# Kernel tuning notes

Hardware: AMD Instinct MI355X
Metric: run time of the kernel (lower is better)

Reference implementation:

```python
import jax, jax.numpy as jnp
import numpy as np
import math

N_HEAD = 12
BLOCK = 256  # local attention block size (ls)
EPS = 1e-6


def _rotate(x):
    # pairs (a, b) -> (-b, a) over last dim (matches rotate_embeddings)
    a = x[..., 0::2]
    b = x[..., 1::2]
    return jnp.stack([-b, a], axis=-1).reshape(x.shape)


def setup_inputs() -> dict:
    key = jax.random.key(0)
    k1, k2, k3 = jax.random.split(key, 3)
    B, T, C = 4, 8192, 768
    s = 0.02
    return {
        "x": jax.random.normal(k1, (B, T, C), jnp.float32),
        "w_qkv": jax.random.normal(k2, (C, 3 * C), jnp.float32) * s,
        "w_ln": jnp.ones((C,), jnp.float32),
        "w_proj": jax.random.normal(k3, (C, C), jnp.float32) * s,
    }


def reference(x, w_qkv, w_ln, w_proj):
    B, T, C = x.shape
    nh, ls = N_HEAD, BLOCK
    hd = C // nh
    ng = T // ls

    xb = x.reshape(B, ng, ls, C)
    qkv = xb @ w_qkv                                   # (B,ng,ls,3C)
    q, k, v = jnp.split(qkv, 3, axis=-1)

    # QK RMSNorm over full embedding dim (before head split)
    def rms(t):
        return t * jax.lax.rsqrt(jnp.mean(t * t, axis=-1, keepdims=True) + EPS) * w_ln
    q, k = rms(q), rms(k)

    # split heads: (B,ng,nh,ls,hd)
    def heads(t):
        return jnp.swapaxes(t.reshape(B, ng, ls, nh, hd), 2, 3)
    q, k, v = heads(q), heads(k), heads(v)

    # RoPE (repo layout: freqs tiled via cat((ts,ts)), interleaved pair rotation)
    pos = 10000.0 ** ((-2.0 * jnp.arange(0, hd, 2, dtype=jnp.float32) - 1.0) / hd)
    ts = jnp.arange(ls, dtype=jnp.float32)[:, None] * pos[None, :]   # (ls, hd/2)
    rot = jnp.concatenate([ts, ts], axis=-1)                          # (ls, hd)
    cos, sin = jnp.cos(rot), jnp.sin(rot)
    q = q * cos + _rotate(q) * sin
    k = k * cos + _rotate(k) * sin

    # block-causal scores: causal only within each local block
    scale = 1.0 / math.sqrt(hd)
    att = jnp.einsum('bgnqd,bgnkd->bgnqk', q, k) * scale              # (B,ng,nh,ls,ls)
    mask = jnp.tril(jnp.ones((ls, ls), dtype=bool))
    att = jnp.where(mask, att, -jnp.finfo(att.dtype).max)
    att = jax.nn.softmax(att, axis=-1)
    y = jnp.einsum('bgnqk,bgnkd->bgnqd', att, v)                      # (B,ng,nh,ls,hd)

    y = jnp.swapaxes(y, 2, 3).reshape(B, ng, ls, C)
    y = y @ w_proj
    return y.reshape(B, T, C)
```

## Files before the change

kernel.cpp:

```cpp
#include <hip/hip_runtime.h>
#include <math.h>

typedef __attribute__((ext_vector_type(8))) short bf16x8;
typedef __attribute__((ext_vector_type(4))) short bf16x4;
typedef __attribute__((ext_vector_type(2))) short bf16x2;
typedef __attribute__((ext_vector_type(4))) float f32x4;
typedef __attribute__((ext_vector_type(16))) float f32x16;

#define NH 12
#define HD 64
#define C0 768
#define C3 2304
#define LS 256
#define KT12 12

static __device__ __forceinline__ float bf2f(short u) {
  union { unsigned int i; float f; } c;
  c.i = ((unsigned int)(unsigned short)u) << 16;
  return c.f;
}
static __device__ __forceinline__ short f2bf(float f) {
  union { float f; unsigned int i; } c; c.f = f;
  unsigned int x = c.i;
  x += 0x7fffu + ((x >> 16) & 1u);
  return (short)(x >> 16);
}
static __device__ __forceinline__ unsigned pk2(float a, float b) {
  return (unsigned)(unsigned short)f2bf(a) | ((unsigned)(unsigned short)f2bf(b) << 16);
}

static __device__ __forceinline__ void gload_lds16(const short* g, const short* l) {
  unsigned long long ga = (unsigned long long)g;
  unsigned int la = (unsigned int)(unsigned long long)l;
  __builtin_amdgcn_global_load_lds(
      (const __attribute__((address_space(1))) void*)ga,
      (__attribute__((address_space(3))) void*)la, 16, 0, 0);
}

__global__ __launch_bounds__(256) void cast_kernel(const float* __restrict__ in,
                                                   short* __restrict__ out, int nquads) {
  int i = blockIdx.x * blockDim.x + threadIdx.x;
  int stride = gridDim.x * blockDim.x;
  for (; i < nquads; i += stride) {
    float4 v = ((const float4*)in)[i];
    bf16x4 o = { f2bf(v.x), f2bf(v.y), f2bf(v.z), f2bf(v.w) };
    ((bf16x4*)out)[i] = o;
  }
}

__global__ __launch_bounds__(256) void cast_transpose_kernel(const float* __restrict__ in,
                                                             short* __restrict__ out,
                                                             int K, int N) {
  __shared__ float tile[32][33];
  int n0 = blockIdx.x * 32, k0 = blockIdx.y * 32;
  int tx = threadIdx.x & 31, ty = threadIdx.x >> 5;
#pragma unroll
  for (int i = 0; i < 32; i += 8)
    tile[ty + i][tx] = in[(long)(k0 + ty + i) * N + n0 + tx];
  __syncthreads();
#pragma unroll
  for (int i = 0; i < 32; i += 8)
    out[(long)(n0 + ty + i) * K + k0 + tx] = f2bf(tile[tx][ty + i]);
}

template <int WNG>
__global__ __launch_bounds__(256) void cast_pack_B_kernel(const float* __restrict__ w,
                                                          short* __restrict__ Bpk, int N) {
  __shared__ short sb[WNG * 64 * 64];
  int bn = blockIdx.x, kt = blockIdx.y, t = threadIdx.x;
#pragma unroll
  for (int i = 0; i < WNG * 2; ++i) {
    int seg = i * 256 + t;
    int k = seg / (WNG * 8);
    int nc = (seg % (WNG * 8)) * 8;
    const float* src = w + ((long)(kt * 64 + k)) * N + bn * (WNG * 64) + nc;
    float4 v0 = *(const float4*)src;
    float4 v1 = *(const float4*)(src + 4);
    sb[(nc + 0) * 64 + k] = f2bf(v0.x); sb[(nc + 1) * 64 + k] = f2bf(v0.y);
    sb[(nc + 2) * 64 + k] = f2bf(v0.z); sb[(nc + 3) * 64 + k] = f2bf(v0.w);
    sb[(nc + 4) * 64 + k] = f2bf(v1.x); sb[(nc + 5) * 64 + k] = f2bf(v1.y);
    sb[(nc + 6) * 64 + k] = f2bf(v1.z); sb[(nc + 7) * 64 + k] = f2bf(v1.w);
  }
  __syncthreads();
#pragma unroll
  for (int i = 0; i < WNG * 2; ++i) {
    int c = i * 256 + t;
    int l = c & 63, f = c >> 6;
    int ks = f & 3, nt = (f >> 2) & 1, wng = f >> 3;
    int col = wng * 64 + nt * 32 + (l & 31);
    int kk = ks * 16 + (l >> 5) * 8;
    bf16x8 v = *(bf16x8*)&sb[col * 64 + kk];
    *(bf16x8*)&Bpk[(((long)bn * KT12 + kt) * (WNG * 512) + c) * 8] = v;
  }
}

__global__ void rope_tab_kernel(float* __restrict__ cost, float* __restrict__ sint) {
  int t = blockIdx.x, d = threadIdx.x;
  int i = d & 31;
  float freq = powf(10000.0f, -(float)(4 * i + 1) / 64.0f);
  float th = (float)t * freq;
  cost[t * 64 + d] = cosf(th);
  sint[t * 64 + d] = sinf(th);
}

#define PH_PRE                                         \
  __builtin_amdgcn_s_barrier();                        \
  __builtin_amdgcn_s_setprio(1);
#define PH_POST                                        \
  __builtin_amdgcn_s_setprio(0);                       \
  asm volatile("s_waitcnt lgkmcnt(0)" ::: "memory");   \
  __builtin_amdgcn_s_barrier();
#define PH_POSTV                                       \
  __builtin_amdgcn_s_setprio(0);                       \
  asm volatile("s_waitcnt lgkmcnt(0)" ::: "memory");   \
  asm volatile("s_waitcnt vmcnt(4)" ::: "memory");     \
  __builtin_amdgcn_s_barrier();
#define MMQ(MH, NP)                                                                \
  { _Pragma("unroll") for (int f_ = 0; f_ < 4; ++f_)                               \
      _Pragma("unroll") for (int n_ = 0; n_ < 2; ++n_)                             \
        _Pragma("unroll") for (int k_ = 0; k_ < 2; ++k_)                           \
          acc[(MH)*4 + f_][(NP)*2 + n_] = __builtin_amdgcn_mfma_f32_16x16x32_bf16( \
              af[f_*2 + k_], bfv[((NP)*2 + n_)*2 + k_],                            \
              acc[(MH)*4 + f_][(NP)*2 + n_], 0, 0, 0); }

template <int OUT_F32>
__global__ __launch_bounds__(512, 2) void gemm8p_kernel(const short* __restrict__ A,
                                                        const short* __restrict__ Bt,
                                                        void* __restrict__ Cout,
                                                        int N, int K, int nbn) {
  __shared__ short lds[65536];
  int t = threadIdx.x, lane = t & 63, wave = t >> 6;
  int lr = lane & 15, lg = lane >> 4;
  int wm = (wave >> 2) * 128, wn = (wave & 3) * 64;
  int id = blockIdx.x;
  int cpx = gridDim.x >> 3;
  int sw = (id & 7) * cpx + (id >> 3);
  int bm = sw / nbn, bn = sw % nbn;
  const short* Abase = A + (long)bm * 256 * K;
  const short* Bbase = Bt + (long)bn * 256 * K;
  int srow = t >> 3;
  int scol = ((t & 7) ^ (srow & 7)) * 8;
  int smax = K >> 4;

  f32x4 acc[8][4];
#pragma unroll
  for (int m = 0; m < 8; ++m)
#pragma unroll
    for (int n = 0; n < 4; ++n) acc[m][n] = (f32x4){0.f, 0.f, 0.f, 0.f};

  bf16x8 af[8], bfv[8];

  auto STAGE = [&](int s) {
    int slot = s & 3;
    int Tg = (s < smax) ? (s >> 2) : 0;
    const short* base = (slot & 2) ? Abase : Bbase;
    const short* g = base + (long)((slot & 1) * 128 + srow) * K + Tg * 64 + scol;
    int lb = ((s >> 2) & 1) * 32768 + ((slot >> 1) ^ 1) * 16384 + (slot & 1) * 8192 + t * 8;
    gload_lds16(g, &lds[lb]);
    gload_lds16(g + (long)64 * K, &lds[lb + 4096]);
  };
  auto LDA = [&](int b, int mh) {
#pragma unroll
    for (int f = 0; f < 4; ++f) {
      int R = wm + mh * 64 + f * 16 + lr;
      int rb = b * 32768 + R * 64;
      int s8 = R & 7;
      af[f * 2 + 0] = *(bf16x8*)&lds[rb + ((lg ^ s8) << 3)];
      af[f * 2 + 1] = *(bf16x8*)&lds[rb + (((4 + lg) ^ s8) << 3)];
    }
  };
  auto LDB = [&](int b, int nh) {
#pragma unroll
    for (int j = 0; j < 2; ++j) {
      int R = wn + (nh * 2 + j) * 16 + lr;
      int rb = b * 32768 + 16384 + R * 64;
      int s8 = R & 7;
      bfv[(nh * 2 + j) * 2 + 0] = *(bf16x8*)&lds[rb + ((lg ^ s8) << 3)];
      bfv[(nh * 2 + j) * 2 + 1] = *(bf16x8*)&lds[rb + (((4 + lg) ^ s8) << 3)];
    }
  };

  STAGE(0); STAGE(1); STAGE(2); STAGE(3); STAGE(4); STAGE(5);
  asm volatile("s_waitcnt vmcnt(4)" ::: "memory");
  __builtin_amdgcn_s_barrier();

  int iters = K >> 7;
  for (int i = 0; i < iters; ++i) {
    int si = 8 * i + 6;
    LDA(0, 0); LDB(0, 0);
    STAGE(si + 0);
    PH_PRE; MMQ(0, 0); PH_POST;
    LDB(0, 1);
    STAGE(si + 1);
    PH_PRE; MMQ(0, 1); PH_POST;
    LDA(0, 1);
    STAGE(si + 2);
    PH_PRE; MMQ(1, 0); PH_POST;
    STAGE(si + 3);
    PH_PRE; MMQ(1, 1); PH_POSTV;
    LDA(1, 0); LDB(1, 0);
    STAGE(si + 4);
    PH_PRE; MMQ(0, 0); PH_POST;
    LDB(1, 1);
    STAGE(si + 5);
    PH_PRE; MMQ(0, 1); PH_POST;
    LDA(1, 1);
    STAGE(si + 6);
    PH_PRE; MMQ(1, 0); PH_POST;
    STAGE(si + 7);
    PH_PRE; MMQ(1, 1); PH_POSTV;
  }

  long crow0 = (long)bm * 256 + wm;
  long ccol0 = (long)bn * 256 + wn;
#pragma unroll
  for (int f = 0; f < 8; ++f)
#pragma unroll
    for (int n = 0; n < 4; ++n)
#pragma unroll
      for (int r = 0; r < 4; ++r) {
        long row = crow0 + (f >> 2) * 64 + (f & 3) * 16 + lg * 4 + r;
        long col = ccol0 + n * 16 + lr;
        float v = acc[f][n][r];
        if (OUT_F32) ((float*)Cout)[row * N + col] = v;
        else ((short*)Cout)[row * N + col] = f2bf(v);
      }
}

template <int OUT_F32>
__global__ __launch_bounds__(256, 2) void gemm128_kernel(const short* __restrict__ Arm,
                                                         const short* __restrict__ Bpk,
                                                         void* __restrict__ Cout,
                                                         int N, int K, int nbn) {
  __shared__ short lds[32768];
  int t = threadIdx.x, lane = t & 63, wave = t >> 6;
  int wm = (wave >> 1) * 64, wng = wave & 1;
  int id = blockIdx.x;
  int cpx = gridDim.x >> 3;
  int sw = (id & 7) * cpx + (id >> 3);
  int bm = sw / nbn, bn = sw % nbn;
  int l31 = lane & 31, lh = lane >> 5;

  f32x16 acc[2][2];
#pragma unroll
  for (int m = 0; m < 2; ++m)
#pragma unroll
    for (int n = 0; n < 2; ++n)
#pragma unroll
      for (int r = 0; r < 16; ++r) acc[m][n][r] = 0.f;

  auto STAGE = [&](int T) {
    int bb = (T & 1) * 16384;
#pragma unroll
    for (int i = 0; i < 4; ++i) {
      int q = i * 256 + t;
      int row = q >> 3, cp = q & 7;
      const short* ga = Arm + ((long)(bm * 128 + row)) * K + T * 64 + ((cp ^ (row & 7)) * 8);
      gload_lds16(ga, &lds[bb + q * 8]);
      const short* gb = Bpk + ((long)bn * KT12 + T) * 8192 + (long)q * 8;
      gload_lds16(gb, &lds[bb + 8192 + q * 8]);
    }
  };

  STAGE(0);
  asm volatile("s_waitcnt vmcnt(0)" ::: "memory");
  __builtin_amdgcn_s_barrier();

  for (int T = 0; T < KT12; ++T) {
    int bb = (T & 1) * 16384;
    if (T + 1 < KT12) STAGE(T + 1);
    bf16x8 a[2][4], b[2][4];
#pragma unroll
    for (int mt = 0; mt < 2; ++mt) {
      int row = wm + mt * 32 + l31;
      int s8 = row & 7;
#pragma unroll
      for (int ks = 0; ks < 4; ++ks) {
        int g = (ks * 2 + lh) ^ s8;
        a[mt][ks] = *(bf16x8*)&lds[bb + row * 64 + g * 8];
      }
    }
#pragma unroll
    for (int nt = 0; nt < 2; ++nt)
#pragma unroll
      for (int ks = 0; ks < 4; ++ks)
        b[nt][ks] = *(bf16x8*)&lds[bb + 8192 + (((wng * 2 + nt) * 4 + ks) * 64 + lane) * 8];
    __builtin_amdgcn_s_setprio(1);
#pragma unroll
    for (int mt = 0; mt < 2; ++mt)
#pragma unroll
      for (int nt = 0; nt < 2; ++nt)
#pragma unroll
        for (int ks = 0; ks < 4; ++ks)
          acc[mt][nt] = __builtin_amdgcn_mfma_f32_32x32x16_bf16(a[mt][ks], b[nt][ks],
                                                                acc[mt][nt], 0, 0, 0);
    __builtin_amdgcn_s_setprio(0);
    asm volatile("s_waitcnt lgkmcnt(0)" ::: "memory");
    asm volatile("s_waitcnt vmcnt(0)" ::: "memory");
    __builtin_amdgcn_s_barrier();
  }

  long crow0 = (long)bm * 128 + wm;
  long ccol0 = (long)bn * 128 + wng * 64;
  int rbase = 4 * lh;
#pragma unroll
  for (int mt = 0; mt < 2; ++mt)
#pragma unroll
    for (int nt = 0; nt < 2; ++nt)
#pragma unroll
      for (int reg = 0; reg < 16; ++reg) {
        long row = crow0 + mt * 32 + (reg & 3) + 8 * (reg >> 2) + rbase;
        long col = ccol0 + nt * 32 + l31;
        float v = acc[mt][nt][reg];
        if (OUT_F32) ((float*)Cout)[row * N + col] = v;
        else ((short*)Cout)[row * N + col] = f2bf(v);
      }
}

__global__ __launch_bounds__(512) void norm_rope_kernel(short* __restrict__ QKV,
    const float* __restrict__ w_ln, const float* __restrict__ cost,
    const float* __restrict__ sint) {
  int wid = (blockIdx.x << 3) + (threadIdx.x >> 6);
  int lane = threadIdx.x & 63;
  int row = wid >> 1;
  int t = row & 255;
  long base = (long)row * C3 + (wid & 1) * C0;
  int e8 = lane * 8, e4 = 512 + lane * 4;
  bf16x8 v8 = *(const bf16x8*)&QKV[base + e8];
  bf16x4 v4 = *(const bf16x4*)&QKV[base + e4];
  float f[12];
#pragma unroll
  for (int j = 0; j < 8; ++j) f[j] = bf2f(v8[j]);
#pragma unroll
  for (int j = 0; j < 4; ++j) f[8 + j] = bf2f(v4[j]);
  float ss = 0.f;
#pragma unroll
  for (int j = 0; j < 12; ++j) ss += f[j] * f[j];
#pragma unroll
  for (int o = 32; o > 0; o >>= 1) ss += __shfl_xor(ss, o);
  float r = rsqrtf(ss * (1.0f / 768.0f) + 1e-6f);
  float4 w0 = *(const float4*)&w_ln[e8];
  float4 w1 = *(const float4*)&w_ln[e8 + 4];
  float4 w2 = *(const float4*)&w_ln[e4];
  float n[12];
  n[0] = f[0] * r * w0.x;  n[1] = f[1] * r * w0.y;
  n[2] = f[2] * r * w0.z;  n[3] = f[3] * r * w0.w;
  n[4] = f[4] * r * w1.x;  n[5] = f[5] * r * w1.y;
  n[6] = f[6] * r * w1.z;  n[7] = f[7] * r * w1.w;
  n[8] = f[8] * r * w2.x;  n[9] = f[9] * r * w2.y;
  n[10] = f[10] * r * w2.z; n[11] = f[11] * r * w2.w;
  int d8 = e8 & 63, d4 = e4 & 63;
  const float* cb = cost + t * 64;
  const float* sbp = sint + t * 64;
  float4 c0 = *(const float4*)&cb[d8], c1 = *(const float4*)&cb[d8 + 4];
  float4 c2 = *(const float4*)&cb[d4];
  float4 s0 = *(const float4*)&sbp[d8], s1 = *(const float4*)&sbp[d8 + 4];
  float4 s2 = *(const float4*)&sbp[d4];
  bf16x8 o8;
  bf16x4 o4;
  o8[0] = f2bf(n[0] * c0.x - n[1] * s0.x);
  o8[1] = f2bf(n[1] * c0.y + n[0] * s0.y);
  o8[2] = f2bf(n[2] * c0.z - n[3] * s0.z);
  o8[3] = f2bf(n[3] * c0.w + n[2] * s0.w);
  o8[4] = f2bf(n[4] * c1.x - n[5] * s1.x);
  o8[5] = f2bf(n[5] * c1.y + n[4] * s1.y);
  o8[6] = f2bf(n[6] * c1.z - n[7] * s1.z);
  o8[7] = f2bf(n[7] * c1.w + n[6] * s1.w);
  o4[0] = f2bf(n[8] * c2.x - n[9] * s2.x);
  o4[1] = f2bf(n[9] * c2.y + n[8] * s2.y);
  o4[2] = f2bf(n[10] * c2.z - n[11] * s2.z);
  o4[3] = f2bf(n[11] * c2.w + n[10] * s2.w);
  *(bf16x8*)&QKV[base + e8] = o8;
  *(bf16x4*)&QKV[base + e4] = o4;
}

__global__ __launch_bounds__(512, 3) void attn_kernel(const short* __restrict__ QKV,
                                                      short* __restrict__ Y) {
  __shared__ short Ks[256 * 64];
  __shared__ short Vt[64 * 256];
  int blk = blockIdx.x;
  int bg = blk / NH, h = blk % NH;
  const long base = (long)bg * LS * C3 + h * HD;
  int tid = threadIdx.x, lane = tid & 63, wave = tid >> 6;
  int lr = lane & 15, lg = lane >> 4;

#pragma unroll
  for (int it = 0; it < 4; ++it) {
    int q = it * 512 + tid;
    int row = q >> 3, cp = q & 7;
    int gcp = cp ^ (row & 7);
    gload_lds16(QKV + base + (long)row * C3 + C0 + gcp * 8, &Ks[q * 8]);
  }
#pragma unroll
  for (int it = 0; it < 8; ++it) {
    int e = tid * 4 + it * 2048;
    int k = e >> 6, n = e & 63;
    bf16x4 v = *(const bf16x4*)&QKV[base + (long)k * C3 + 2 * C0 + n];
#pragma unroll
    for (int j = 0; j < 4; ++j) {
      int nn = n + j;
      Vt[nn * 256 + (((k >> 3) ^ (nn & 7)) << 3) + (k & 7)] = v[j];
    }
  }
  asm volatile("s_waitcnt vmcnt(0)" ::: "memory");
  __syncthreads();

  int addrA = (((lane >> 4) & 1) * 32 + lr) * 4;
  int addrB = addrA + 64;
  bool selhi = (lane & 32) != 0;

  for (int tt = 0; tt < 2; ++tt) {
    int tile = (tt == 0) ? wave : (15 - wave);
    int m0 = tile * 16;
    bf16x8 qf[2];
#pragma unroll
    for (int ks = 0; ks < 2; ++ks)
      qf[ks] = *(const bf16x8*)&QKV[base + (long)(m0 + lr) * C3 + ks * 32 + lg * 8];

    f32x4 zero4 = {0.f, 0.f, 0.f, 0.f};
    f32x4 accs[16];
#pragma unroll
    for (int n = 0; n < 16; ++n) accs[n] = zero4;

    __builtin_amdgcn_s_setprio(1);
#pragma unroll
    for (int n = 0; n < 16; ++n) {
      if (n <= tile) {
        int row = n * 16 + lr, sw = row & 7;
        bf16x8 k0 = *(bf16x8*)&Ks[row * 64 + ((lg ^ sw) << 3)];
        bf16x8 k1 = *(bf16x8*)&Ks[row * 64 + (((4 + lg) ^ sw) << 3)];
        accs[n] = __builtin_amdgcn_mfma_f32_16x16x32_bf16(k0, qf[0], accs[n], 0, 0, 0);
        accs[n] = __builtin_amdgcn_mfma_f32_16x16x32_bf16(k1, qf[1], accs[n], 0, 0, 0);
      }
    }
    __builtin_amdgcn_s_setprio(0);

    float tm[16];
#pragma unroll
    for (int n = 0; n < 16; ++n) {
      if (n <= tile) {
        if (n == tile) {
#pragma unroll
          for (int r = 0; r < 4; ++r)
            accs[n][r] = (lg * 4 + r <= lr) ? accs[n][r] : -1e30f;
        }
        float m01 = fmaxf(accs[n][0], accs[n][1]);
        float m23 = fmaxf(accs[n][2], accs[n][3]);
        tm[n] = fmaxf(m01, m23);
      } else {
        tm[n] = -1e30f;
      }
    }
#pragma unroll
    for (int st = 1; st < 16; st <<= 1)
#pragma unroll
      for (int j = 0; j < 16; j += 2 * st) tm[j] = fmaxf(tm[j], tm[j + st]);
    float mloc = tm[0];
    mloc = fmaxf(mloc, __shfl_xor(mloc, 16));
    mloc = fmaxf(mloc, __shfl_xor(mloc, 32));

    float ts[16];
#pragma unroll
    for (int n = 0; n < 16; ++n) {
      if (n <= tile) {
#pragma unroll
        for (int r = 0; r < 4; ++r) accs[n][r] = __expf((accs[n][r] - mloc) * 0.125f);
        float s01 = accs[n][0] + accs[n][1];
        float s23 = accs[n][2] + accs[n][3];
        ts[n] = s01 + s23;
      } else {
        ts[n] = 0.f;
      }
    }
#pragma unroll
    for (int st = 1; st < 16; st <<= 1)
#pragma unroll
      for (int j = 0; j < 16; j += 2 * st) ts[j] += ts[j + st];
    float s = ts[0];
    s += __shfl_xor(s, 16);
    s += __shfl_xor(s, 32);
    float rs = 1.0f / s;
    float rv[4];
#pragma unroll
    for (int r = 0; r < 4; ++r) {
      union { float f; int i; } c; c.f = rs;
      union { int i; float f; } o;
      o.i = __builtin_amdgcn_ds_bpermute((lg * 4 + r) * 4, c.i);
      rv[r] = o.f;
    }

    int ktmax = (m0 + 15) >> 5;
    f32x4 yacc[4];
#pragma unroll
    for (int n2 = 0; n2 < 4; ++n2) yacc[n2] = zero4;
#pragma unroll
    for (int kt = 0; kt < 8; ++kt) {
      if (kt <= ktmax) {
        int n0 = 2 * kt, n1 = 2 * kt + 1;
        unsigned a01_0 = pk2(accs[n0][0], accs[n0][1]);
        unsigned a23_0 = pk2(accs[n0][2], accs[n0][3]);
        unsigned a01_1 = (n1 <= tile) ? pk2(accs[n1][0], accs[n1][1]) : 0u;
        unsigned a23_1 = (n1 <= tile) ? pk2(accs[n1][2], accs[n1][3]) : 0u;
        union { unsigned u[4]; bf16x8 v; } af;
        unsigned g0a = (unsigned)__builtin_amdgcn_ds_bpermute(addrA, (int)a01_0);
        unsigned g0b = (unsigned)__builtin_amdgcn_ds_bpermute(addrA, (int)a01_1);
        unsigned g1a = (unsigned)__builtin_amdgcn_ds_bpermute(addrA, (int)a23_0);
        unsigned g1b = (unsigned)__builtin_amdgcn_ds_bpermute(addrA, (int)a23_1);
        unsigned g2a = (unsigned)__builtin_amdgcn_ds_bpermute(addrB, (int)a01_0);
        unsigned g2b = (unsigned)__builtin_amdgcn_ds_bpermute(addrB, (int)a01_1);
        unsigned g3a = (unsigned)__builtin_amdgcn_ds_bpermute(addrB, (int)a23_0);
        unsigned g3b = (unsigned)__builtin_amdgcn_ds_bpermute(addrB, (int)a23_1);
        af.u[0] = selhi ? g0b : g0a;
        af.u[1] = selhi ? g1b : g1a;
        af.u[2] = selhi ? g2b : g2a;
        af.u[3] = selhi ? g3b : g3a;
        int ac = kt * 32 + lg * 8;
        __builtin_amdgcn_s_setprio(1);
#pragma unroll
        for (int n2 = 0; n2 < 4; ++n2) {
          int vn = n2 * 16 + lr;
          bf16x8 vb = *(bf16x8*)&Vt[vn * 256 + (((ac >> 3) ^ (vn & 7)) << 3)];
          yacc[n2] = __builtin_amdgcn_mfma_f32_16x16x32_bf16(af.v, vb, yacc[n2], 0, 0, 0);
        }
        __builtin_amdgcn_s_setprio(0);
      }
    }

#pragma unroll
    for (int n2 = 0; n2 < 4; ++n2) {
#pragma unroll
      for (int r = 0; r < 4; ++r) {
        int row = m0 + lg * 4 + r, d = n2 * 16 + lr;
        Y[((long)(bg * LS + row)) * C0 + h * HD + d] = f2bf(yacc[n2][r] * rv[r]);
      }
    }
  }
}

extern "C" void kernel_launch(void* const* d_in, const int* in_sizes, int n_in,
                              void* d_out, int out_size, void* d_ws, size_t ws_size,
                              hipStream_t stream) {
  (void)in_sizes; (void)n_in; (void)out_size; (void)ws_size;
  const float* x = (const float*)d_in[0];
  const float* w_qkv = (const float*)d_in[1];
  const float* w_ln = (const float*)d_in[2];
  const float* w_proj = (const float*)d_in[3];
  float* out = (float*)d_out;

  char* ws = (char*)d_ws;
  short* Xb      = (short*)(ws + 0);
  short* QKV     = (short*)(ws + 50331648);
  short* Yb      = (short*)(ws + 201326592);
  short* WqkvT   = (short*)(ws + 251658240);
  short* WprojPk = (short*)(ws + 255197184);
  float* cost    = (float*)(ws + 256376832);
  float* sint    = (float*)(ws + 256442368);

  cast_kernel<<<2048, 256, 0, stream>>>(x, Xb, (4 * 8192 * C0) / 4);
  cast_transpose_kernel<<<dim3(C3 / 32, C0 / 32), 256, 0, stream>>>(w_qkv, WqkvT, C0, C3);
  cast_pack_B_kernel<2><<<dim3(6, KT12), 256, 0, stream>>>(w_proj, WprojPk, C0);
  rope_tab_kernel<<<256, 64, 0, stream>>>(cost, sint);

  gemm8p_kernel<0><<<(C3 / 256) * (32768 / 256), 512, 0, stream>>>(Xb, WqkvT, QKV,
                                                                   C3, C0, C3 / 256);
  norm_rope_kernel<<<8192, 512, 0, stream>>>(QKV, w_ln, cost, sint);
  attn_kernel<<<128 * NH, 512, 0, stream>>>(QKV, Yb);
  gemm128_kernel<1><<<256 * 6, 256, 0, stream>>>(Yb, WprojPk, out, C0, C0, 6);
}
```

Before: 316.3 us.

## Use packed-B gemm128 for QKV and drop softmax max subtraction

New measurement: 318.7 us. About the same (+0.8%).

```diff
diff --git a/kernel.cpp b/kernel.cpp
--- a/kernel.cpp
+++ b/kernel.cpp
@@ -3,7 +3,6 @@
 
 typedef __attribute__((ext_vector_type(8))) short bf16x8;
 typedef __attribute__((ext_vector_type(4))) short bf16x4;
-typedef __attribute__((ext_vector_type(2))) short bf16x2;
 typedef __attribute__((ext_vector_type(4))) float f32x4;
 typedef __attribute__((ext_vector_type(16))) float f32x16;
 
@@ -46,21 +45,6 @@
     bf16x4 o = { f2bf(v.x), f2bf(v.y), f2bf(v.z), f2bf(v.w) };
     ((bf16x4*)out)[i] = o;
   }
-}
-
-__global__ __launch_bounds__(256) void cast_transpose_kernel(const float* __restrict__ in,
-                                                             short* __restrict__ out,
-                                                             int K, int N) {
-  __shared__ float tile[32][33];
-  int n0 = blockIdx.x * 32, k0 = blockIdx.y * 32;
-  int tx = threadIdx.x & 31, ty = threadIdx.x >> 5;
-#pragma unroll
-  for (int i = 0; i < 32; i += 8)
-    tile[ty + i][tx] = in[(long)(k0 + ty + i) * N + n0 + tx];
-  __syncthreads();
-#pragma unroll
-  for (int i = 0; i < 32; i += 8)
-    out[(long)(n0 + ty + i) * K + k0 + tx] = f2bf(tile[tx][ty + i]);
 }
 
 template <int WNG>
@@ -101,130 +85,6 @@
   float th = (float)t * freq;
   cost[t * 64 + d] = cosf(th);
   sint[t * 64 + d] = sinf(th);
-}
-
-#define PH_PRE                                         \
-  __builtin_amdgcn_s_barrier();                        \
-  __builtin_amdgcn_s_setprio(1);
-#define PH_POST                                        \
-  __builtin_amdgcn_s_setprio(0);                       \
-  asm volatile("s_waitcnt lgkmcnt(0)" ::: "memory");   \
-  __builtin_amdgcn_s_barrier();
-#define PH_POSTV                                       \
-  __builtin_amdgcn_s_setprio(0);                       \
-  asm volatile("s_waitcnt lgkmcnt(0)" ::: "memory");   \
-  asm volatile("s_waitcnt vmcnt(4)" ::: "memory");     \
-  __builtin_amdgcn_s_barrier();
-#define MMQ(MH, NP)                                                                \
-  { _Pragma("unroll") for (int f_ = 0; f_ < 4; ++f_)                               \
-      _Pragma("unroll") for (int n_ = 0; n_ < 2; ++n_)                             \
-        _Pragma("unroll") for (int k_ = 0; k_ < 2; ++k_)                           \
-          acc[(MH)*4 + f_][(NP)*2 + n_] = __builtin_amdgcn_mfma_f32_16x16x32_bf16( \
-              af[f_*2 + k_], bfv[((NP)*2 + n_)*2 + k_],                            \
-              acc[(MH)*4 + f_][(NP)*2 + n_], 0, 0, 0); }
-
-template <int OUT_F32>
-__global__ __launch_bounds__(512, 2) void gemm8p_kernel(const short* __restrict__ A,
-                                                        const short* __restrict__ Bt,
-                                                        void* __restrict__ Cout,
-                                                        int N, int K, int nbn) {
-  __shared__ short lds[65536];
-  int t = threadIdx.x, lane = t & 63, wave = t >> 6;
-  int lr = lane & 15, lg = lane >> 4;
-  int wm = (wave >> 2) * 128, wn = (wave & 3) * 64;
-  int id = blockIdx.x;
-  int cpx = gridDim.x >> 3;
-  int sw = (id & 7) * cpx + (id >> 3);
-  int bm = sw / nbn, bn = sw % nbn;
-  const short* Abase = A + (long)bm * 256 * K;
-  const short* Bbase = Bt + (long)bn * 256 * K;
-  int srow = t >> 3;
-  int scol = ((t & 7) ^ (srow & 7)) * 8;
-  int smax = K >> 4;
-
-  f32x4 acc[8][4];
-#pragma unroll
-  for (int m = 0; m < 8; ++m)
-#pragma unroll
-    for (int n = 0; n < 4; ++n) acc[m][n] = (f32x4){0.f, 0.f, 0.f, 0.f};
-
-  bf16x8 af[8], bfv[8];
-
-  auto STAGE = [&](int s) {
-    int slot = s & 3;
-    int Tg = (s < smax) ? (s >> 2) : 0;
-    const short* base = (slot & 2) ? Abase : Bbase;
-    const short* g = base + (long)((slot & 1) * 128 + srow) * K + Tg * 64 + scol;
-    int lb = ((s >> 2) & 1) * 32768 + ((slot >> 1) ^ 1) * 16384 + (slot & 1) * 8192 + t * 8;
-    gload_lds16(g, &lds[lb]);
-    gload_lds16(g + (long)64 * K, &lds[lb + 4096]);
-  };
-  auto LDA = [&](int b, int mh) {
-#pragma unroll
-    for (int f = 0; f < 4; ++f) {
-      int R = wm + mh * 64 + f * 16 + lr;
-      int rb = b * 32768 + R * 64;
-      int s8 = R & 7;
-      af[f * 2 + 0] = *(bf16x8*)&lds[rb + ((lg ^ s8) << 3)];
-      af[f * 2 + 1] = *(bf16x8*)&lds[rb + (((4 + lg) ^ s8) << 3)];
-    }
-  };
-  auto LDB = [&](int b, int nh) {
-#pragma unroll
-    for (int j = 0; j < 2; ++j) {
-      int R = wn + (nh * 2 + j) * 16 + lr;
-      int rb = b * 32768 + 16384 + R * 64;
-      int s8 = R & 7;
-      bfv[(nh * 2 + j) * 2 + 0] = *(bf16x8*)&lds[rb + ((lg ^ s8) << 3)];
-      bfv[(nh * 2 + j) * 2 + 1] = *(bf16x8*)&lds[rb + (((4 + lg) ^ s8) << 3)];
-    }
-  };
-
-  STAGE(0); STAGE(1); STAGE(2); STAGE(3); STAGE(4); STAGE(5);
-  asm volatile("s_waitcnt vmcnt(4)" ::: "memory");
-  __builtin_amdgcn_s_barrier();
-
-  int iters = K >> 7;
-  for (int i = 0; i < iters; ++i) {
-    int si = 8 * i + 6;
-    LDA(0, 0); LDB(0, 0);
-    STAGE(si + 0);
-    PH_PRE; MMQ(0, 0); PH_POST;
-    LDB(0, 1);
-    STAGE(si + 1);
-    PH_PRE; MMQ(0, 1); PH_POST;
-    LDA(0, 1);
-    STAGE(si + 2);
-    PH_PRE; MMQ(1, 0); PH_POST;
-    STAGE(si + 3);
-    PH_PRE; MMQ(1, 1); PH_POSTV;
-    LDA(1, 0); LDB(1, 0);
-    STAGE(si + 4);
-    PH_PRE; MMQ(0, 0); PH_POST;
-    LDB(1, 1);
-    STAGE(si + 5);
-    PH_PRE; MMQ(0, 1); PH_POST;
-    LDA(1, 1);
-    STAGE(si + 6);
-    PH_PRE; MMQ(1, 0); PH_POST;
-    STAGE(si + 7);
-    PH_PRE; MMQ(1, 1); PH_POSTV;
-  }
-
-  long crow0 = (long)bm * 256 + wm;
-  long ccol0 = (long)bn * 256 + wn;
-#pragma unroll
-  for (int f = 0; f < 8; ++f)
-#pragma unroll
-    for (int n = 0; n < 4; ++n)
-#pragma unroll
-      for (int r = 0; r < 4; ++r) {
-        long row = crow0 + (f >> 2) * 64 + (f & 3) * 16 + lg * 4 + r;
-        long col = ccol0 + n * 16 + lr;
-        float v = acc[f][n][r];
-        if (OUT_F32) ((float*)Cout)[row * N + col] = v;
-        else ((short*)Cout)[row * N + col] = f2bf(v);
-      }
 }
 
 template <int OUT_F32>
@@ -435,7 +295,7 @@
     }
     __builtin_amdgcn_s_setprio(0);
 
-    float tm[16];
+    float ts[16];
 #pragma unroll
     for (int n = 0; n < 16; ++n) {
       if (n <= tile) {
@@ -444,27 +304,8 @@
           for (int r = 0; r < 4; ++r)
             accs[n][r] = (lg * 4 + r <= lr) ? accs[n][r] : -1e30f;
         }
-        float m01 = fmaxf(accs[n][0], accs[n][1]);
-        float m23 = fmaxf(accs[n][2], accs[n][3]);
-        tm[n] = fmaxf(m01, m23);
-      } else {
-        tm[n] = -1e30f;
-      }
-    }
-#pragma unroll
-    for (int st = 1; st < 16; st <<= 1)
-#pragma unroll
-      for (int j = 0; j < 16; j += 2 * st) tm[j] = fmaxf(tm[j], tm[j + st]);
-    float mloc = tm[0];
-    mloc = fmaxf(mloc, __shfl_xor(mloc, 16));
-    mloc = fmaxf(mloc, __shfl_xor(mloc, 32));
-
-    float ts[16];
-#pragma unroll
-    for (int n = 0; n < 16; ++n) {
-      if (n <= tile) {
-#pragma unroll
-        for (int r = 0; r < 4; ++r) accs[n][r] = __expf((accs[n][r] - mloc) * 0.125f);
+#pragma unroll
+        for (int r = 0; r < 4; ++r) accs[n][r] = __expf(accs[n][r] * 0.125f);
         float s01 = accs[n][0] + accs[n][1];
         float s23 = accs[n][2] + accs[n][3];
         ts[n] = s01 + s23;
@@ -551,18 +392,17 @@
   short* Xb      = (short*)(ws + 0);
   short* QKV     = (short*)(ws + 50331648);
   short* Yb      = (short*)(ws + 201326592);
-  short* WqkvT   = (short*)(ws + 251658240);
+  short* WqkvPk  = (short*)(ws + 251658240);
   short* WprojPk = (short*)(ws + 255197184);
   float* cost    = (float*)(ws + 256376832);
   float* sint    = (float*)(ws + 256442368);
 
   cast_kernel<<<2048, 256, 0, stream>>>(x, Xb, (4 * 8192 * C0) / 4);
-  cast_transpose_kernel<<<dim3(C3 / 32, C0 / 32), 256, 0, stream>>>(w_qkv, WqkvT, C0, C3);
+  cast_pack_B_kernel<2><<<dim3(18, KT12), 256, 0, stream>>>(w_qkv, WqkvPk, C3);
   cast_pack_B_kernel<2><<<dim3(6, KT12), 256, 0, stream>>>(w_proj, WprojPk, C0);
   rope_tab_kernel<<<256, 64, 0, stream>>>(cost, sint);
 
-  gemm8p_kernel<0><<<(C3 / 256) * (32768 / 256), 512, 0, stream>>>(Xb, WqkvT, QKV,
-                                                                   C3, C0, C3 / 256);
+  gemm128_kernel<0><<<256 * 18, 256, 0, stream>>>(Xb, WqkvPk, QKV, C3, C0, 18);
   norm_rope_kernel<<<8192, 512, 0, stream>>>(QKV, w_ln, cost, sint);
   attn_kernel<<<128 * NH, 512, 0, stream>>>(QKV, Yb);
   gemm128_kernel<1><<<256 * 6, 256, 0, stream>>>(Yb, WprojPk, out, C0, C0, 6);
```
